# Performance work log

Hardware: AMD Instinct MI355X
Metric: run time of the kernel (lower is better)

The kernel has to match this reference:

```python
import jax, jax.numpy as jnp
import numpy as np

B, Z, K, T = 4, 64, 400, 48000
CIN, COUT, KS, DIL = 128, 128, 3, 1
H = 32


def setup_inputs() -> dict:
    key = jax.random.key(0)
    ks = jax.random.split(key, 10)
    s = lambda n: 1.0 / np.sqrt(n)
    return {
        "x": jax.random.normal(ks[0], (B, CIN, T), jnp.float32),
        "z": jax.random.normal(ks[1], (B, Z, K), jnp.float32),
        # weight_model: Conv1d(Z->H, k=1), ReLU, Conv1d(H -> CIN*COUT*KS, k=1)
        "w1": jax.random.normal(ks[2], (H, Z), jnp.float32) * s(Z),
        "b1": jax.random.normal(ks[3], (H,), jnp.float32) * 0.01,
        "w2": jax.random.normal(ks[4], (CIN * COUT * KS, H), jnp.float32) * s(H),
        "b2": jax.random.normal(ks[5], (CIN * COUT * KS,), jnp.float32) * s(CIN * KS),
        # bias_model: Conv1d(Z->H, k=1), ReLU, Conv1d(H -> COUT, k=1)
        "bw1": jax.random.normal(ks[6], (H, Z), jnp.float32) * s(Z),
        "bb1": jax.random.normal(ks[7], (H,), jnp.float32) * 0.01,
        "bw2": jax.random.normal(ks[8], (COUT, H), jnp.float32) * s(H),
        "bb2": jax.random.normal(ks[9], (COUT,), jnp.float32) * 0.01,
    }


def _mlp1x1(z, wa, ba, wb, bb):
    # two pointwise Conv1d layers with ReLU in between; z: [B, Z, K]
    h = jax.nn.relu(jnp.einsum('hz,bzk->bhk', wa, z) + ba[None, :, None])
    return jnp.einsum('oh,bhk->bok', wb, h) + bb[None, :, None]


def _unfold_causal(x, ksize, dil):
    # causal im2col: tap i is x delayed by i*dil samples (left-padded with zeros)
    pad = dil * (ksize - 1)
    xp = jnp.pad(x, ((0, 0), (0, 0), (pad, 0)))
    taps = [xp[:, :, pad - i * dil: pad - i * dil + x.shape[-1]] for i in range(ksize)]
    return jnp.concatenate(taps, axis=1)  # [B, CIN*KS, T]


def reference(x, z, w1, b1, w2, b2, bw1, bb1, bw2, bb2):
    Tk = T // K  # samples per weight chunk
    xu = _unfold_causal(x, KS, DIL)                       # [B, CIN*KS, T]
    xr = xu.transpose(0, 2, 1).reshape(B * K, Tk, CIN * KS)
    w = _mlp1x1(z, w1, b1, w2, b2)                        # [B, CIN*COUT*KS, K]
    w = w.reshape(B, CIN * KS, COUT, K).transpose(0, 3, 1, 2).reshape(B * K, CIN * KS, COUT)
    bias = _mlp1x1(z, bw1, bb1, bw2, bb2)                 # [B, COUT, K]
    bias = bias.transpose(0, 2, 1).reshape(B * K, COUT)
    y = jnp.einsum('btc,bco->bto', xr, w) + bias[:, None, :]
    return y.reshape(B, T, COUT).transpose(0, 2, 1)       # [B, COUT, T]
```

## Files before the change

### kernel.cpp

```cpp
#include <hip/hip_runtime.h>
#include <stdint.h>

#define TT     48000
#define TK     120
#define NC     128
#define NA     384
#define NZ     64
#define NH     32
#define NK     400
#define NCHUNK 1600
#define MW     49152
#define XROWS  48002

typedef float f32x4 __attribute__((ext_vector_type(4)));
typedef __bf16 bf16x8 __attribute__((ext_vector_type(8)));

static __device__ __forceinline__ uint16_t f2bf(float f) {
    uint32_t x; __builtin_memcpy(&x, &f, 4);
    return (uint16_t)((x + 0x7fffu + ((x >> 16) & 1u)) >> 16);
}
static __device__ __forceinline__ uint32_t pk2(uint16_t lo, uint16_t hi) {
    return (uint32_t)lo | ((uint32_t)hi << 16);
}

__global__ __launch_bounds__(256) void k0w(
    const float* __restrict__ w2, const float* __restrict__ b2,
    uint16_t* __restrict__ w2p, float* __restrict__ b2p) {
    int m = blockIdx.x * 256 + threadIdx.x;
    int a = m >> 7, c = m & 127;
    int mp = c * NA + a;
    const float* src = w2 + (size_t)m * NH;
    uint16_t* dst = w2p + (size_t)mp * NH;
#pragma unroll
    for (int i = 0; i < NH; i += 8) {
        float4 v0 = *(const float4*)(src + i);
        float4 v1 = *(const float4*)(src + i + 4);
        uint4 o;
        o.x = pk2(f2bf(v0.x), f2bf(v0.y));
        o.y = pk2(f2bf(v0.z), f2bf(v0.w));
        o.z = pk2(f2bf(v1.x), f2bf(v1.y));
        o.w = pk2(f2bf(v1.z), f2bf(v1.w));
        *(uint4*)(dst + i) = o;
    }
    b2p[mp] = b2[m];
}

__global__ __launch_bounds__(256) void k0x(
    const float* __restrict__ x, uint16_t* __restrict__ Xt) {
    int t0 = blockIdx.x * 128, cin0 = blockIdx.y * 64, b = blockIdx.z;
    int tid = threadIdx.x;
    __shared__ __align__(16) uint16_t Lt[128][72];
    const float* xb = x + ((size_t)b * NC + cin0) * TT + t0;
    int cg = (tid & 7) * 8;
    int tq = (tid >> 3) * 4;
    uint16_t vb[4][8];
#pragma unroll
    for (int i = 0; i < 8; ++i) {
        float4 v = *(const float4*)(xb + (size_t)(cg + i) * TT + tq);
        vb[0][i] = f2bf(v.x); vb[1][i] = f2bf(v.y);
        vb[2][i] = f2bf(v.z); vb[3][i] = f2bf(v.w);
    }
#pragma unroll
    for (int j = 0; j < 4; ++j) {
        uint4 o; __builtin_memcpy(&o, vb[j], 16);
        *(uint4*)&Lt[tq + j][cg] = o;
    }
    __syncthreads();
    uint16_t* XtB = Xt + (size_t)b * XROWS * NC;
#pragma unroll
    for (int r = 0; r < 4; ++r) {
        int s = r * 256 + tid;
        int t = s >> 3, cc = s & 7;
        uint4 o = *(uint4*)&Lt[t][cc * 8];
        *(uint4*)(XtB + (size_t)(t0 + t + 2) * NC + cin0 + cc * 8) = o;
    }
    if (blockIdx.x == 0 && blockIdx.y == 0 && tid < 32)
        *(uint4*)(XtB + tid * 8) = make_uint4(0, 0, 0, 0);
}

__global__ __launch_bounds__(256) void k1_hidden(
    const float* __restrict__ z,
    const float* __restrict__ w1, const float* __restrict__ b1,
    const float* __restrict__ bw1, const float* __restrict__ bb1,
    const float* __restrict__ bw2, const float* __restrict__ bb2,
    uint16_t* __restrict__ Hb, float* __restrict__ biasws) {
    int tid = threadIdx.x, lane = tid & 63, w = tid >> 6;
    int chunk0 = blockIdx.x * 4;
    int b = chunk0 / NK;
    int k0 = chunk0 - b * NK;

    __shared__ float w1sT[64][33];
    __shared__ float bw1sT[64][33];
    __shared__ float bw2s[128][33];
    __shared__ float zs[64][4];
    __shared__ float hbs[4][33];
    __shared__ float b1s[32], bb1s[32], bb2s[128];

    {
        int row = tid >> 3, c0 = (tid & 7) * 8;
        float4 a0 = *(const float4*)(w1 + row * NZ + c0);
        float4 a1 = *(const float4*)(w1 + row * NZ + c0 + 4);
        float4 c0v = *(const float4*)(bw1 + row * NZ + c0);
        float4 c1v = *(const float4*)(bw1 + row * NZ + c0 + 4);
        const float av[8] = {a0.x,a0.y,a0.z,a0.w,a1.x,a1.y,a1.z,a1.w};
        const float cv[8] = {c0v.x,c0v.y,c0v.z,c0v.w,c1v.x,c1v.y,c1v.z,c1v.w};
#pragma unroll
        for (int j = 0; j < 8; ++j) {
            w1sT[c0 + j][row]  = av[j];
            bw1sT[c0 + j][row] = cv[j];
        }
    }
    {
        int r = tid >> 1, cb = (tid & 1) * 16;
        float4 v0 = *(const float4*)(bw2 + r * NH + cb);
        float4 v1 = *(const float4*)(bw2 + r * NH + cb + 4);
        float4 v2 = *(const float4*)(bw2 + r * NH + cb + 8);
        float4 v3 = *(const float4*)(bw2 + r * NH + cb + 12);
        const float vv[16] = {v0.x,v0.y,v0.z,v0.w,v1.x,v1.y,v1.z,v1.w,
                              v2.x,v2.y,v2.z,v2.w,v3.x,v3.y,v3.z,v3.w};
#pragma unroll
        for (int j = 0; j < 16; ++j) bw2s[r][cb + j] = vv[j];
    }
    if (tid < 64) {
        float4 zv = *(const float4*)(z + ((size_t)b * NZ + tid) * NK + k0);
        zs[tid][0] = zv.x; zs[tid][1] = zv.y; zs[tid][2] = zv.z; zs[tid][3] = zv.w;
    }
    if (tid < 32) { b1s[tid] = b1[tid]; bb1s[tid] = bb1[tid]; }
    if (tid >= 128 && tid < 256) bb2s[tid - 128] = bb2[tid - 128];
    __syncthreads();

    int chunk = chunk0 + w;
    if (lane < NH) {
        float s = b1s[lane];
#pragma unroll
        for (int i = 0; i < NZ; ++i) s = fmaf(w1sT[i][lane], zs[i][w], s);
        Hb[(size_t)chunk * NH + lane] = f2bf(fmaxf(s, 0.f));
    } else {
        int j = lane - NH;
        float s = bb1s[j];
#pragma unroll
        for (int i = 0; i < NZ; ++i) s = fmaf(bw1sT[i][j], zs[i][w], s);
        hbs[w][j] = fmaxf(s, 0.f);
    }

#pragma unroll
    for (int r = 0; r < 2; ++r) {
        int c = r * 64 + lane;
        float s = bb2s[c];
#pragma unroll
        for (int j = 0; j < NH; ++j) s = fmaf(bw2s[c][j], hbs[w][j], s);
        biasws[(size_t)chunk * NC + c] = s;
    }
}

__global__ __launch_bounds__(256) void k2_wgen(
    const uint16_t* __restrict__ w2p, const float* __restrict__ b2p,
    const uint16_t* __restrict__ Hb, uint16_t* __restrict__ Wt,
    int chunk0, int nchunk) {
    int tid = threadIdx.x, lane = tid & 63, w = tid >> 6;
    int quad = lane >> 4, li = lane & 15;
    __shared__ __align__(16) uint16_t St[4][16][264];

    int clocal = blockIdx.y * 16 + li;
    int cl = clocal < nchunk ? clocal : (nchunk - 1);
    bf16x8 bfrag = *(const bf16x8*)(Hb + (size_t)(chunk0 + cl) * NH + quad * 8);
    int mbase = blockIdx.x * 1024 + w * 256;

#pragma unroll
    for (int t = 0; t < 16; ++t) {
        int mb = mbase + t * 16;
        bf16x8 afrag = *(const bf16x8*)(w2p + (size_t)(mb + li) * NH + quad * 8);
        f32x4 acc = {0.f, 0.f, 0.f, 0.f};
        acc = __builtin_amdgcn_mfma_f32_16x16x32_bf16(afrag, bfrag, acc, 0, 0, 0);
        float4 bias = *(const float4*)(b2p + mb + quad * 4);
        uint16_t p[4] = { f2bf(acc[0] + bias.x), f2bf(acc[1] + bias.y),
                          f2bf(acc[2] + bias.z), f2bf(acc[3] + bias.w) };
        uint64_t pv; __builtin_memcpy(&pv, p, 8);
        *(uint64_t*)&St[w][li][t * 16 + quad * 4] = pv;
    }
#pragma unroll
    for (int p = 0; p < 8; ++p) {
        int ch = (lane >> 4) + (p & 3) * 4;
        int part = lane & 15, mh = p >> 2;
        uint4 v = *(const uint4*)&St[w][ch][mh * 128 + part * 8];
        int cg = blockIdx.y * 16 + ch;
        if (cg < nchunk)
            *(uint4*)(Wt + (size_t)cg * MW + mbase + mh * 128 + part * 8) = v;
    }
}

__global__ __launch_bounds__(256) void k3_conv(
    const uint16_t* __restrict__ Xt, const uint16_t* __restrict__ Wt,
    const float* __restrict__ biasws, float* __restrict__ out, int chunk0) {
    int cl = blockIdx.x, chunk = chunk0 + cl;
    int b = chunk / NK, k = chunk - b * NK;
    int kbase = k * TK;
    int tid = threadIdx.x, lane = tid & 63, w = tid >> 6;
    int quad = lane >> 4, li = lane & 15;
    int tblk = (w & 1) * 64, cblk = (w >> 1) * 64;

    __shared__ __align__(16) char smem[32768];
    char* As = smem;
    char* Ws = smem + 16384;
    const uint16_t* XtB = Xt + (size_t)b * XROWS * NC;
    const uint16_t* WtC = Wt + (size_t)cl * MW;

    f32x4 acc[4][4];
#pragma unroll
    for (int i = 0; i < 4; ++i)
#pragma unroll
        for (int j = 0; j < 4; ++j) acc[i][j] = (f32x4){0.f, 0.f, 0.f, 0.f};

#pragma unroll
    for (int dk = 0; dk < 6; ++dk) {
        int a0 = dk * 64, tap = a0 >> 7, cin0 = a0 & 127;
#pragma unroll
        for (int i = 0; i < 4; ++i) {
            int kc = 2 * w + (i >> 1), half = i & 1;
            int t = half * 64 + lane;
            const uint16_t* g = XtB + (size_t)(kbase + t - tap + 2) * NC + cin0 + kc * 8;
            __builtin_amdgcn_global_load_lds(
                (__attribute__((address_space(1))) void*)g,
                (__attribute__((address_space(3))) void*)(As + kc * 2048 + half * 1024),
                16, 0, 0);
        }
#pragma unroll
        for (int i = 0; i < 4; ++i) {
            int kc = 2 * w + (i >> 1), half = i & 1;
            int c = half * 64 + lane;
            const uint16_t* g = WtC + (size_t)c * NA + a0 + kc * 8;
            __builtin_amdgcn_global_load_lds(
                (__attribute__((address_space(1))) void*)g,
                (__attribute__((address_space(3))) void*)(Ws + kc * 2048 + half * 1024),
                16, 0, 0);
        }
        __syncthreads();
#pragma unroll
        for (int s = 0; s < 2; ++s) {
            bf16x8 af[4], bfr[4];
#pragma unroll
            for (int tt = 0; tt < 4; ++tt)
                af[tt] = *(const bf16x8*)(As + (s * 4 + quad) * 2048 + (tblk + tt * 16 + li) * 16);
#pragma unroll
            for (int ct = 0; ct < 4; ++ct)
                bfr[ct] = *(const bf16x8*)(Ws + (s * 4 + quad) * 2048 + (cblk + ct * 16 + li) * 16);
#pragma unroll
            for (int tt = 0; tt < 4; ++tt)
#pragma unroll
                for (int ct = 0; ct < 4; ++ct)
                    acc[tt][ct] = __builtin_amdgcn_mfma_f32_16x16x32_bf16(
                        af[tt], bfr[ct], acc[tt][ct], 0, 0, 0);
        }
        __syncthreads();
    }

#pragma unroll
    for (int ct = 0; ct < 4; ++ct) {
        int c = cblk + ct * 16 + li;
        float bias = biasws[(size_t)chunk * NC + c];
        float* ob = out + ((size_t)b * NC + c) * TT + kbase;
#pragma unroll
        for (int tt = 0; tt < 4; ++tt) {
            int t0v = tblk + tt * 16 + quad * 4;
            if (t0v < TK) {
                f32x4 v = acc[tt][ct];
                *(float4*)(ob + t0v) = make_float4(v[0] + bias, v[1] + bias,
                                                   v[2] + bias, v[3] + bias);
            }
        }
    }
}

extern "C" void kernel_launch(void* const* d_in, const int* in_sizes, int n_in,
                              void* d_out, int out_size, void* d_ws, size_t ws_size,
                              hipStream_t stream) {
    const float* x   = (const float*)d_in[0];
    const float* z   = (const float*)d_in[1];
    const float* w1  = (const float*)d_in[2];
    const float* b1  = (const float*)d_in[3];
    const float* w2  = (const float*)d_in[4];
    const float* b2  = (const float*)d_in[5];
    const float* bw1 = (const float*)d_in[6];
    const float* bb1 = (const float*)d_in[7];
    const float* bw2 = (const float*)d_in[8];
    const float* bb2 = (const float*)d_in[9];
    float* out = (float*)d_out;

    char* ws = (char*)d_ws;
    uint16_t* Hb     = (uint16_t*)(ws);
    float*    biasws = (float*)(ws + 102400);
    uint16_t* w2p    = (uint16_t*)(ws + 921600);
    float*    b2p    = (float*)(ws + 4067328);
    uint16_t* Xt     = (uint16_t*)(ws + 4263936);
    const size_t wt_off = 53422080;
    uint16_t* Wt     = (uint16_t*)(ws + wt_off);

    size_t avail = (ws_size > wt_off) ? (ws_size - wt_off) : 0;
    int batch = (int)(avail / ((size_t)MW * 2));
    if (batch > 800) batch = 800;
    if (batch < 1) batch = 1;

    k0w<<<MW / 256, 256, 0, stream>>>(w2, b2, w2p, b2p);
    k0x<<<dim3(TT / 128, 2, 4), 256, 0, stream>>>(x, Xt);
    k1_hidden<<<NCHUNK / 4, 256, 0, stream>>>(z, w1, b1, bw1, bb1, bw2, bb2, Hb, biasws);

    for (int c0 = 0; c0 < NCHUNK; c0 += batch) {
        int nc = NCHUNK - c0;
        if (nc > batch) nc = batch;
        dim3 g2(MW / 1024, (nc + 15) / 16, 1);
        k2_wgen<<<g2, 256, 0, stream>>>(w2p, b2p, Hb, Wt, c0, nc);
        k3_conv<<<nc, 256, 0, stream>>>(Xt, Wt, biasws, out, c0);
    }
}
```

Baseline: 324.4 us.

## Fuse per-chunk weight generation into the convolution kernel via LDS

Replaces the two-kernel scheme (generate per-chunk bf16 weights into a large global workspace, then run the conv GEMM) with one fused kernel. Each block covers 8 chunks and 16 output channels. It generates that weight slice with MFMA directly into a swizzled LDS buffer and immediately consumes it, reading the input activations straight from global memory instead of staging them in LDS. This removes roughly 157 MB of weight writes and reads plus the batching loop and launches. In exchange, the MFMA work for half of each weight tile is wasted (li<8 only), and X rows are re-read by each of 8 channel-group blocks.

```diff
diff --git a/kernel.cpp b/kernel.cpp
--- a/kernel.cpp
+++ b/kernel.cpp
@@ -153,120 +153,84 @@
     }
 }
 
-__global__ __launch_bounds__(256) void k2_wgen(
+__global__ __launch_bounds__(256, 2) void k23_fused(
     const uint16_t* __restrict__ w2p, const float* __restrict__ b2p,
-    const uint16_t* __restrict__ Hb, uint16_t* __restrict__ Wt,
-    int chunk0, int nchunk) {
+    const uint16_t* __restrict__ Hb, const uint16_t* __restrict__ Xt,
+    const float* __restrict__ biasws, float* __restrict__ out) {
     int tid = threadIdx.x, lane = tid & 63, w = tid >> 6;
     int quad = lane >> 4, li = lane & 15;
-    __shared__ __align__(16) uint16_t St[4][16][264];
-
-    int clocal = blockIdx.y * 16 + li;
-    int cl = clocal < nchunk ? clocal : (nchunk - 1);
-    bf16x8 bfrag = *(const bf16x8*)(Hb + (size_t)(chunk0 + cl) * NH + quad * 8);
-    int mbase = blockIdx.x * 1024 + w * 256;
-
-#pragma unroll
-    for (int t = 0; t < 16; ++t) {
-        int mb = mbase + t * 16;
-        bf16x8 afrag = *(const bf16x8*)(w2p + (size_t)(mb + li) * NH + quad * 8);
-        f32x4 acc = {0.f, 0.f, 0.f, 0.f};
-        acc = __builtin_amdgcn_mfma_f32_16x16x32_bf16(afrag, bfrag, acc, 0, 0, 0);
-        float4 bias = *(const float4*)(b2p + mb + quad * 4);
-        uint16_t p[4] = { f2bf(acc[0] + bias.x), f2bf(acc[1] + bias.y),
-                          f2bf(acc[2] + bias.z), f2bf(acc[3] + bias.w) };
-        uint64_t pv; __builtin_memcpy(&pv, p, 8);
-        *(uint64_t*)&St[w][li][t * 16 + quad * 4] = pv;
-    }
-#pragma unroll
-    for (int p = 0; p < 8; ++p) {
-        int ch = (lane >> 4) + (p & 3) * 4;
-        int part = lane & 15, mh = p >> 2;
-        uint4 v = *(const uint4*)&St[w][ch][mh * 128 + part * 8];
-        int cg = blockIdx.y * 16 + ch;
-        if (cg < nchunk)
-            *(uint4*)(Wt + (size_t)cg * MW + mbase + mh * 128 + part * 8) = v;
-    }
-}
-
-__global__ __launch_bounds__(256) void k3_conv(
-    const uint16_t* __restrict__ Xt, const uint16_t* __restrict__ Wt,
-    const float* __restrict__ biasws, float* __restrict__ out, int chunk0) {
-    int cl = blockIdx.x, chunk = chunk0 + cl;
-    int b = chunk / NK, k = chunk - b * NK;
-    int kbase = k * TK;
-    int tid = threadIdx.x, lane = tid & 63, w = tid >> 6;
-    int quad = lane >> 4, li = lane & 15;
-    int tblk = (w & 1) * 64, cblk = (w >> 1) * 64;
-
-    __shared__ __align__(16) char smem[32768];
-    char* As = smem;
-    char* Ws = smem + 16384;
+    int gx = blockIdx.x;
+    int gy = blockIdx.y;
+    int chunk0 = gx * 8;
+    int b = chunk0 / NK;
+    int kb0 = (chunk0 - b * NK) * TK;
+    int c0 = gy * 16;
+    size_t m0 = (size_t)c0 * NA;
+
+    __shared__ __align__(16) uint16_t Wlds[8][24][16][8];
+
+    bf16x8 hfrag = *(const bf16x8*)(Hb + (size_t)(chunk0 + (li & 7)) * NH + quad * 8);
     const uint16_t* XtB = Xt + (size_t)b * XROWS * NC;
-    const uint16_t* WtC = Wt + (size_t)cl * MW;
-
-    f32x4 acc[4][4];
-#pragma unroll
-    for (int i = 0; i < 4; ++i)
-#pragma unroll
-        for (int j = 0; j < 4; ++j) acc[i][j] = (f32x4){0.f, 0.f, 0.f, 0.f};
-
-#pragma unroll
-    for (int dk = 0; dk < 6; ++dk) {
-        int a0 = dk * 64, tap = a0 >> 7, cin0 = a0 & 127;
-#pragma unroll
-        for (int i = 0; i < 4; ++i) {
-            int kc = 2 * w + (i >> 1), half = i & 1;
-            int t = half * 64 + lane;
-            const uint16_t* g = XtB + (size_t)(kbase + t - tap + 2) * NC + cin0 + kc * 8;
-            __builtin_amdgcn_global_load_lds(
-                (__attribute__((address_space(1))) void*)g,
-                (__attribute__((address_space(3))) void*)(As + kc * 2048 + half * 1024),
-                16, 0, 0);
-        }
-#pragma unroll
-        for (int i = 0; i < 4; ++i) {
-            int kc = 2 * w + (i >> 1), half = i & 1;
-            int c = half * 64 + lane;
-            const uint16_t* g = WtC + (size_t)c * NA + a0 + kc * 8;
-            __builtin_amdgcn_global_load_lds(
-                (__attribute__((address_space(1))) void*)g,
-                (__attribute__((address_space(3))) void*)(Ws + kc * 2048 + half * 1024),
-                16, 0, 0);
+
+    f32x4 acc[8][2];
+#pragma unroll
+    for (int i = 0; i < 8; ++i) {
+        acc[i][0] = (f32x4){0.f, 0.f, 0.f, 0.f};
+        acc[i][1] = (f32x4){0.f, 0.f, 0.f, 0.f};
+    }
+    int tb = w * 32;
+
+#pragma unroll
+    for (int p = 0; p < 2; ++p) {
+        if (p) __syncthreads();
+#pragma unroll
+        for (int j = 0; j < 48; ++j) {
+            int mt = j * 4 + w;
+            int cl = mt / 12;
+            int al = (mt % 12) * 16;
+            bf16x8 afrag = *(const bf16x8*)(
+                w2p + (m0 + (size_t)cl * NA + p * 192 + al + li) * NH + quad * 8);
+            f32x4 z4 = {0.f, 0.f, 0.f, 0.f};
+            f32x4 d = __builtin_amdgcn_mfma_f32_16x16x32_bf16(afrag, hfrag, z4, 0, 0, 0);
+            float4 bias = *(const float4*)(b2p + m0 + cl * NA + p * 192 + al + quad * 4);
+            if (li < 8) {
+                uint16_t pk[4] = { f2bf(d[0] + bias.x), f2bf(d[1] + bias.y),
+                                   f2bf(d[2] + bias.z), f2bf(d[3] + bias.w) };
+                uint64_t pv; __builtin_memcpy(&pv, pk, 8);
+                *(uint64_t*)&Wlds[li][(al >> 3) + (quad >> 1)][cl ^ li][(quad & 1) * 4] = pv;
+            }
         }
         __syncthreads();
 #pragma unroll
-        for (int s = 0; s < 2; ++s) {
-            bf16x8 af[4], bfr[4];
-#pragma unroll
-            for (int tt = 0; tt < 4; ++tt)
-                af[tt] = *(const bf16x8*)(As + (s * 4 + quad) * 2048 + (tblk + tt * 16 + li) * 16);
-#pragma unroll
-            for (int ct = 0; ct < 4; ++ct)
-                bfr[ct] = *(const bf16x8*)(Ws + (s * 4 + quad) * 2048 + (cblk + ct * 16 + li) * 16);
-#pragma unroll
-            for (int tt = 0; tt < 4; ++tt)
-#pragma unroll
-                for (int ct = 0; ct < 4; ++ct)
-                    acc[tt][ct] = __builtin_amdgcn_mfma_f32_16x16x32_bf16(
-                        af[tt], bfr[ct], acc[tt][ct], 0, 0, 0);
-        }
-        __syncthreads();
-    }
-
-#pragma unroll
-    for (int ct = 0; ct < 4; ++ct) {
-        int c = cblk + ct * 16 + li;
-        float bias = biasws[(size_t)chunk * NC + c];
-        float* ob = out + ((size_t)b * NC + c) * TT + kbase;
-#pragma unroll
-        for (int tt = 0; tt < 4; ++tt) {
-            int t0v = tblk + tt * 16 + quad * 4;
-            if (t0v < TK) {
-                f32x4 v = acc[tt][ct];
-                *(float4*)(ob + t0v) = make_float4(v[0] + bias, v[1] + bias,
-                                                   v[2] + bias, v[3] + bias);
+        for (int ch = 0; ch < 8; ++ch) {
+            const uint16_t* row0 = XtB + (size_t)(kb0 + ch * TK + tb + li + 2) * NC;
+#pragma unroll
+            for (int s = 0; s < 6; ++s) {
+                int ag = p * 192 + s * 32 + quad * 8;
+                int off = (ag & 127) - (ag >> 7) * NC;
+                bf16x8 bfr = *(const bf16x8*)&Wlds[ch][s * 4 + quad][li ^ ch][0];
+                bf16x8 a0 = *(const bf16x8*)(row0 + off);
+                bf16x8 a1 = *(const bf16x8*)(row0 + 16 * NC + off);
+                acc[ch][0] = __builtin_amdgcn_mfma_f32_16x16x32_bf16(a0, bfr, acc[ch][0], 0, 0, 0);
+                acc[ch][1] = __builtin_amdgcn_mfma_f32_16x16x32_bf16(a1, bfr, acc[ch][1], 0, 0, 0);
             }
+        }
+    }
+
+    int cg = c0 + li;
+    int t0 = tb + quad * 4;
+#pragma unroll
+    for (int ch = 0; ch < 8; ++ch) {
+        int chunk = chunk0 + ch;
+        float bias = biasws[(size_t)chunk * NC + cg];
+        float* ob = out + ((size_t)b * NC + cg) * TT + kb0 + ch * TK;
+        f32x4 v0 = acc[ch][0];
+        *(float4*)(ob + t0) = make_float4(v0[0] + bias, v0[1] + bias,
+                                          v0[2] + bias, v0[3] + bias);
+        if (t0 + 16 < TK) {
+            f32x4 v1 = acc[ch][1];
+            *(float4*)(ob + t0 + 16) = make_float4(v1[0] + bias, v1[1] + bias,
+                                                   v1[2] + bias, v1[3] + bias);
         }
     }
 }
@@ -292,23 +256,9 @@
     uint16_t* w2p    = (uint16_t*)(ws + 921600);
     float*    b2p    = (float*)(ws + 4067328);
     uint16_t* Xt     = (uint16_t*)(ws + 4263936);
-    const size_t wt_off = 53422080;
-    uint16_t* Wt     = (uint16_t*)(ws + wt_off);
-
-    size_t avail = (ws_size > wt_off) ? (ws_size - wt_off) : 0;
-    int batch = (int)(avail / ((size_t)MW * 2));
-    if (batch > 800) batch = 800;
-    if (batch < 1) batch = 1;
 
     k0w<<<MW / 256, 256, 0, stream>>>(w2, b2, w2p, b2p);
     k0x<<<dim3(TT / 128, 2, 4), 256, 0, stream>>>(x, Xt);
     k1_hidden<<<NCHUNK / 4, 256, 0, stream>>>(z, w1, b1, bw1, bb1, bw2, bb2, Hb, biasws);
-
-    for (int c0 = 0; c0 < NCHUNK; c0 += batch) {
-        int nc = NCHUNK - c0;
-        if (nc > batch) nc = batch;
-        dim3 g2(MW / 1024, (nc + 15) / 16, 1);
-        k2_wgen<<<g2, 256, 0, stream>>>(w2p, b2p, Hb, Wt, c0, nc);
-        k3_conv<<<nc, 256, 0, stream>>>(Xt, Wt, biasws, out, c0);
-    }
-}
+    k23_fused<<<dim3(200, 8), 256, 0, stream>>>(w2p, b2p, Hb, Xt, biasws, out);
+}
```

Measured after the change: 812.6 us. +150.5%, slower.

## Load X time-slab once into swizzled LDS and reuse across conv taps

Applied to the files above, without the earlier changes.

The X activation tile for a chunk is now staged into LDS once as a 128-row by 128-channel slab with an XOR swizzle, instead of being reloaded from global memory for every tap and K-slice. The three causal taps are served by row-shifted reads from that single slab, with clamping at the tile edge. This cuts redundant global traffic for X and is meant to reduce LDS bank conflicts. In exchange the LDS footprint grows from 32 KB to 48 KB, which may lower occupancy. The weight slices are still loaded per step, with an extra barrier between steps.

```diff
diff --git a/kernel.cpp b/kernel.cpp
--- a/kernel.cpp
+++ b/kernel.cpp
@@ -199,9 +199,9 @@
     int quad = lane >> 4, li = lane & 15;
     int tblk = (w & 1) * 64, cblk = (w >> 1) * 64;
 
-    __shared__ __align__(16) char smem[32768];
-    char* As = smem;
-    char* Ws = smem + 16384;
+    __shared__ __align__(16) char smem[49152];
+    char* Xa = smem;
+    char* Ws = smem + 32768;
     const uint16_t* XtB = Xt + (size_t)b * XROWS * NC;
     const uint16_t* WtC = Wt + (size_t)cl * MW;
 
@@ -212,18 +212,18 @@
         for (int j = 0; j < 4; ++j) acc[i][j] = (f32x4){0.f, 0.f, 0.f, 0.f};
 
 #pragma unroll
-    for (int dk = 0; dk < 6; ++dk) {
-        int a0 = dk * 64, tap = a0 >> 7, cin0 = a0 & 127;
-#pragma unroll
-        for (int i = 0; i < 4; ++i) {
-            int kc = 2 * w + (i >> 1), half = i & 1;
-            int t = half * 64 + lane;
-            const uint16_t* g = XtB + (size_t)(kbase + t - tap + 2) * NC + cin0 + kc * 8;
-            __builtin_amdgcn_global_load_lds(
-                (__attribute__((address_space(1))) void*)g,
-                (__attribute__((address_space(3))) void*)(As + kc * 2048 + half * 1024),
-                16, 0, 0);
-        }
+    for (int i = 0; i < 8; ++i) {
+        int brow = w * 32 + i * 4 + quad;
+        const uint16_t* g = XtB + (size_t)(kbase + brow) * NC
+                          + ((li ^ (brow & 15)) * 8);
+        __builtin_amdgcn_global_load_lds(
+            (__attribute__((address_space(1))) void*)g,
+            (__attribute__((address_space(3))) void*)(Xa + (w * 32 + i * 4) * 256),
+            16, 0, 0);
+    }
+
+    {
+        int a0 = 0;
 #pragma unroll
         for (int i = 0; i < 4; ++i) {
             int kc = 2 * w + (i >> 1), half = i & 1;
@@ -234,13 +234,22 @@
                 (__attribute__((address_space(3))) void*)(Ws + kc * 2048 + half * 1024),
                 16, 0, 0);
         }
-        __syncthreads();
+    }
+    __syncthreads();
+
+#pragma unroll
+    for (int dk = 0; dk < 6; ++dk) {
+        int tap = dk >> 1;
 #pragma unroll
         for (int s = 0; s < 2; ++s) {
             bf16x8 af[4], bfr[4];
 #pragma unroll
-            for (int tt = 0; tt < 4; ++tt)
-                af[tt] = *(const bf16x8*)(As + (s * 4 + quad) * 2048 + (tblk + tt * 16 + li) * 16);
+            for (int tt = 0; tt < 4; ++tt) {
+                int r = tblk + tt * 16 + li + 2 - tap;
+                r = r > 127 ? 127 : r;
+                int q = (dk & 1) * 8 + s * 4 + quad;
+                af[tt] = *(const bf16x8*)(Xa + r * 256 + ((q ^ (r & 15)) << 4));
+            }
 #pragma unroll
             for (int ct = 0; ct < 4; ++ct)
                 bfr[ct] = *(const bf16x8*)(Ws + (s * 4 + quad) * 2048 + (cblk + ct * 16 + li) * 16);
@@ -252,6 +261,20 @@
                         af[tt], bfr[ct], acc[tt][ct], 0, 0, 0);
         }
         __syncthreads();
+        if (dk < 5) {
+            int a0 = (dk + 1) * 64;
+#pragma unroll
+            for (int i = 0; i < 4; ++i) {
+                int kc = 2 * w + (i >> 1), half = i & 1;
+                int c = half * 64 + lane;
+                const uint16_t* g = WtC + (size_t)c * NA + a0 + kc * 8;
+                __builtin_amdgcn_global_load_lds(
+                    (__attribute__((address_space(1))) void*)g,
+                    (__attribute__((address_space(3))) void*)(Ws + kc * 2048 + half * 1024),
+                    16, 0, 0);
+            }
+            __syncthreads();
+        }
     }
 
 #pragma unroll
```

Result: faster. 310.0 us (-4.4%).
